# Performance work log

Measured on AMD Instinct MI355X. Metric: run time of the kernel, lower is better.

## Reference

```python
import jax, jax.numpy as jnp
import numpy as np

T, B, I = 64, 128, 512   # seq_len, batch, input_size
H = 512                   # hidden_size
Z = 512                   # zhidden_size (== H required by cell_fn math)
A = 3                     # n_axis
L = 4 + 1                 # n_hidden_layer + 1 levels per Multi_LSTM


def setup_inputs() -> dict:
    key = jax.random.key(0)
    ks = jax.random.split(key, 9)
    s = 0.03  # xavier-ish scale for 512-dim layers
    x = jax.random.normal(ks[0], (T, B, I), jnp.float32)
    # Multi_LSTM cell weights per axis/level: 4 gates (i,f,g,o).
    Wx = jax.random.normal(ks[1], (A, L, 4, H, H), jnp.float32) * s
    Wh = jax.random.normal(ks[2], (A, L, 4, H, H), jnp.float32) * s
    b_lstm = jnp.zeros((A, L, 4, H), jnp.float32)  # b_i + b_h (both init zero)
    # cell_fn (inp_w) weights per level/axis: 3 gates (i,f,c) + combine Wilc.
    Wg_h = jax.random.normal(ks[3], (L, A, 3, Z, H), jnp.float32) * s
    Wg_p = jax.random.normal(ks[4], (L, A, 3, Z, Z), jnp.float32) * s
    bg = jnp.zeros((L, A, 3, Z), jnp.float32)
    Wilc = jax.random.normal(ks[5], (L, A, Z, Z), jnp.float32) * s
    bilc = jnp.zeros((L, A, Z), jnp.float32)
    # single_li: em_size (= L*Z) -> hidden_size
    Wsl = jax.random.normal(ks[6], (H, L * Z), jnp.float32) * s
    bsl = jnp.zeros((H,), jnp.float32)
    # per-timestep linear: hidden_size -> 1 (ModuleList over seq_len)
    Wlin = jax.random.normal(ks[7], (T, 1, H), jnp.float32) * s
    blin = jnp.zeros((T, 1), jnp.float32)
    return dict(x=x, Wx=Wx, Wh=Wh, b_lstm=b_lstm, Wg_h=Wg_h, Wg_p=Wg_p, bg=bg,
                Wilc=Wilc, bilc=bilc, Wsl=Wsl, bsl=bsl, Wlin=Wlin, blin=blin)


def _forward(x, Wx, Wh, b_lstm, Wg_h, Wg_p, bg, Wilc, bilc, Wsl, bsl, Wlin, blin):
    Tn, Bn, _ = x.shape
    An, Ln = Wx.shape[0], Wx.shape[1]
    Hn, Zn = Wx.shape[3], Wilc.shape[2]

    def step(carry, inp_t):
        h_g, hs, cs = carry          # h_g: (B,H); hs,cs: (L,A,B,H)
        xt, wl, bl = inp_t
        # --- per-axis stacked LSTM (Multi_LSTM), levels sequential ---
        inp = jnp.broadcast_to(xt[None], (An, Bn, Hn))
        new_h, new_c = [], []
        for l in range(Ln):
            pre = (jnp.einsum('abi,agoi->abgo', inp, Wx[:, l])
                   + jnp.einsum('abi,agoi->abgo', hs[l], Wh[:, l])
                   + b_lstm[:, l][:, None])           # (A,B,4,H)
            i = jax.nn.sigmoid(pre[:, :, 0]); f = jax.nn.sigmoid(pre[:, :, 1])
            g = jnp.tanh(pre[:, :, 2]);      o = jax.nn.sigmoid(pre[:, :, 3])
            c = f * cs[l] + i * g
            h = o * jnp.tanh(c)
            new_h.append(h); new_c.append(c)
            inp = h
        sh = jnp.stack(new_h)        # (L,A,B,H)
        sc = jnp.stack(new_c)        # (L,A,B,H)
        # --- cell_fn per level, vectorized over levels and axes ---
        pre = (jnp.einsum('bh,lagzh->labgz', h_g, Wg_h)
               + jnp.einsum('labz,lagyz->labgy', sh, Wg_p)
               + bg[:, :, None])                      # (L,A,B,3,Z)
        i = jax.nn.sigmoid(pre[..., 0, :])
        f = jax.nn.sigmoid(pre[..., 1, :])
        g = jnp.tanh(pre[..., 2, :])
        i_cell = i * sc
        c_cell = f * g + i_cell
        # NOTE: torch code uses Wt_1/bt_1 for BOTH t_1 and t_2 (repo bug kept).
        t1 = jnp.einsum('labz,lazy->laby', i_cell, Wilc) + bilc[:, :, None]
        t2 = jnp.einsum('labz,lazy->laby', c_cell, Wilc) + bilc[:, :, None]
        comb = jax.nn.sigmoid(t2.sum(1)) * jax.nn.softmax(t1.sum(1), axis=-1)  # (L,B,Z)
        cat = jnp.transpose(comb, (1, 0, 2)).reshape(Bn, Ln * Zn)
        h_new = cat @ Wsl.T + bsl                      # single_li
        y = h_new @ wl.T + bl                          # per-step linear -> (B,1)
        return (h_new, sh, sc), y

    carry0 = (jnp.zeros((Bn, Hn), x.dtype),
              jnp.zeros((Ln, An, Bn, Hn), x.dtype),
              jnp.zeros((Ln, An, Bn, Hn), x.dtype))
    _, ys = jax.lax.scan(step, carry0, (x, Wlin, blin))
    return ys  # (T,B,1)


def reference(x, Wx, Wh, b_lstm, Wg_h, Wg_p, bg, Wilc, bilc, Wsl, bsl, Wlin, blin):
    return _forward(x, Wx, Wh, b_lstm, Wg_h, Wg_p, bg, Wilc, bilc, Wsl, bsl, Wlin, blin)
```

## Files before the change

kernel.cpp:

```cpp
#include <hip/hip_runtime.h>
#include <cstdint>

typedef __bf16 bf16;
typedef bf16 bf16x8 __attribute__((ext_vector_type(8)));
typedef bf16 bf16x4 __attribute__((ext_vector_type(4)));
typedef float f32x4 __attribute__((ext_vector_type(4)));

#define DI __device__ __forceinline__

DI float sigmoidf_(float x) { return 1.0f / (1.0f + __expf(-x)); }
DI float tanhf_(float x)    { return 1.0f - 2.0f / (__expf(2.0f * x) + 1.0f); }

DI void gld16(const void* g, void* l) {
  __builtin_amdgcn_global_load_lds(
      (const __attribute__((address_space(1))) void*)g,
      (__attribute__((address_space(3))) void*)l, 16, 0, 0);
}

template<int SE>
DI void stage128(char* ldsb, const bf16* act, int k0, int wave, int lane)
{
  const int rsub = lane >> 3, s = lane & 7;
#pragma unroll
  for (int j = 0; j < 4; ++j) {
    const int r = (wave * 4 + j) * 8 + rsub;
    gld16(act + (long)r * SE + k0 + ((s ^ (r & 7)) << 3),
          ldsb + (wave * 4 + j) * 1024);
  }
}

template<int SE>
DI void stage64x2(char* ldsb, const bf16* a1, const bf16* a2, int k0,
                  int wave, int lane)
{
  const int rsub = lane >> 3, s = lane & 7;
#pragma unroll
  for (int j = 0; j < 2; ++j) {
    const int r = (wave * 2 + j) * 8 + rsub;
    const long go = (long)r * SE + k0 + ((s ^ (r & 7)) << 3);
    gld16(a1 + go, ldsb + (wave * 2 + j) * 1024);
    gld16(a2 + go, ldsb + 8192 + (wave * 2 + j) * 1024);
  }
}

DI bf16x8 ldsAf(const char* p, int r, int m)
{
  return *(const bf16x8*)(p + r * 128 + ((m ^ (r & 7)) << 4));
}

template<int NB, int K, int STRIDE>
DI void mmK(f32x4* acc, const bf16* __restrict__ wrow,
            const bf16* __restrict__ act, int q, int col)
{
#pragma unroll
  for (int ki = 0; ki < K / 32; ++ki) {
    const int k = ki * 32 + q * 8;
    bf16x8 wf = *(const bf16x8*)(wrow + k);
#pragma unroll
    for (int bt = 0; bt < NB; ++bt) {
      bf16x8 af = *(const bf16x8*)(act + (long)(bt * 16 + col) * STRIDE + k);
      acc[bt] = __builtin_amdgcn_mfma_f32_16x16x32_bf16(wf, af, acc[bt], 0, 0, 0);
    }
  }
}

DI void d_lstm(int bid, int tid, char* smem,
               const bf16* __restrict__ A0, long a0ss,
               const bf16* __restrict__ A1,
               const bf16* __restrict__ W,
               const float* __restrict__ bias,
               const float* __restrict__ csR,
               float* __restrict__ csW,
               bf16* __restrict__ hOut)
{
  const int bx = bid & 31, ax = bid >> 5;
  const int lane = tid & 63, wave = tid >> 6;
  const int q = lane >> 4, col = lane & 15;
  const int n0 = bx * 64 + wave * 16;
  const bf16* wrow = W + (long)ax * 10485760L + (long)(n0 + col) * 1024;
  const bf16* a0 = A0 + (long)ax * a0ss;
  const bf16* a1 = A1 + (long)ax * 65536;
  f32x4 acc[8] = {};
  stage128<512>(smem, a0, 0, wave, lane);
  __syncthreads();
#pragma unroll 2
  for (int c = 0; c < 16; ++c) {
    if (c < 15) {
      const bf16* an = ((c + 1) < 8) ? a0 : a1;
      stage128<512>(smem + (((c + 1) & 1) << 14), an, ((c + 1) & 7) * 64,
                    wave, lane);
    }
    const char* p = smem + ((c & 1) << 14);
#pragma unroll
    for (int ki = 0; ki < 2; ++ki) {
      bf16x8 wf = *(const bf16x8*)(wrow + c * 64 + ki * 32 + q * 8);
#pragma unroll
      for (int bt = 0; bt < 8; ++bt)
        acc[bt] = __builtin_amdgcn_mfma_f32_16x16x32_bf16(
            wf, ldsAf(p, bt * 16 + col, ki * 4 + q), acc[bt], 0, 0, 0);
    }
    __syncthreads();
  }
  const int o = (n0 >> 2) + q;
  const float* bi = bias + (long)ax * 10240;
  float b0f = bi[o], b1f = bi[512 + o], b2f = bi[1024 + o], b3f = bi[1536 + o];
  const float* csr = csR + (long)ax * 65536;
  float* csw = csW + (long)ax * 65536;
  bf16* hl = hOut + (long)ax * 65536;
#pragma unroll
  for (int bt = 0; bt < 8; ++bt) {
    int b = bt * 16 + col;
    float ig = sigmoidf_(acc[bt][0] + b0f);
    float fg = sigmoidf_(acc[bt][1] + b1f);
    float gg = tanhf_   (acc[bt][2] + b2f);
    float og = sigmoidf_(acc[bt][3] + b3f);
    long idx = (long)b * 512 + o;
    float cn = fg * csr[idx] + ig * gg;
    csw[idx] = cn;
    hl[idx] = (bf16)(og * tanhf_(cn));
  }
}

DI void d_cell(int bid, int tid, char* smem,
               const bf16* __restrict__ hg, const bf16* __restrict__ hsC,
               const bf16* __restrict__ Wg, const float* __restrict__ bgp,
               const float* __restrict__ csC,
               bf16* __restrict__ icat, bf16* __restrict__ ccat)
{
  const int bx = bid & 31, sl = bid >> 5;
  const int l = sl / 3, a = sl - l * 3;
  const int lane = tid & 63, wave = tid >> 6;
  const int q = lane >> 4, col = lane & 15;
  const int n0 = bx * 64 + wave * 16;
  const bf16* wrow = Wg + (long)sl * 2097152L + (long)(n0 + col) * 1024;
  const bf16* a0 = hg;
  const bf16* a1 = hsC + (long)sl * 65536;
  f32x4 acc[8] = {};
  stage128<512>(smem, a0, 0, wave, lane);
  __syncthreads();
#pragma unroll 2
  for (int c = 0; c < 16; ++c) {
    if (c < 15) {
      const bf16* an = ((c + 1) < 8) ? a0 : a1;
      stage128<512>(smem + (((c + 1) & 1) << 14), an, ((c + 1) & 7) * 64,
                    wave, lane);
    }
    const char* p = smem + ((c & 1) << 14);
#pragma unroll
    for (int ki = 0; ki < 2; ++ki) {
      bf16x8 wf = *(const bf16x8*)(wrow + c * 64 + ki * 32 + q * 8);
#pragma unroll
      for (int bt = 0; bt < 8; ++bt)
        acc[bt] = __builtin_amdgcn_mfma_f32_16x16x32_bf16(
            wf, ldsAf(p, bt * 16 + col, ki * 4 + q), acc[bt], 0, 0, 0);
    }
    __syncthreads();
  }
  const int z = (n0 >> 2) + q;
  const float* bgl = bgp + (long)sl * 1536;
  float g0 = bgl[z], g1 = bgl[512 + z], g2 = bgl[1024 + z];
  const float* csl = csC + (long)sl * 65536;
  const long obase = (long)l * 196608 + (long)a * 512 + z;
#pragma unroll
  for (int bt = 0; bt < 8; ++bt) {
    int b = bt * 16 + col;
    float ig = sigmoidf_(acc[bt][0] + g0);
    float fg = sigmoidf_(acc[bt][1] + g1);
    float gg = tanhf_   (acc[bt][2] + g2);
    float sc = csl[(long)b * 512 + z];
    float icl = ig * sc;
    float ccl = fg * gg + icl;
    long oi = obase + (long)b * 1536;
    icat[oi] = (bf16)icl;
    ccat[oi] = (bf16)ccl;
  }
}

DI void d_tg(int bid, int tid, char* smem,
             const bf16* __restrict__ icat, const bf16* __restrict__ ccat,
             const bf16* __restrict__ Wt, const float* __restrict__ bilc,
             float* __restrict__ t1s, float* __restrict__ t2s)
{
  const int bx = bid & 7, by = (bid >> 3) & 1, l = bid >> 4;
  const int lane = tid & 63, wave = tid >> 6;
  const int q = lane >> 4, col = lane & 15;
  const int n0 = bx * 64 + wave * 16;
  const int b0 = by * 64;
  const bf16* wrow = Wt + (long)l * 786432L + (long)(n0 + col) * 1536;
  const bf16* ic = icat + (long)l * 196608 + (long)b0 * 1536;
  const bf16* cc = ccat + (long)l * 196608 + (long)b0 * 1536;
  f32x4 a1[4] = {}, a2[4] = {};
  stage64x2<1536>(smem, ic, cc, 0, wave, lane);
  __syncthreads();
#pragma unroll 2
  for (int c = 0; c < 24; ++c) {
    if (c < 23)
      stage64x2<1536>(smem + (((c + 1) & 1) << 14), ic, cc, (c + 1) * 64,
                      wave, lane);
    const char* p = smem + ((c & 1) << 14);
#pragma unroll
    for (int ki = 0; ki < 2; ++ki) {
      bf16x8 wf = *(const bf16x8*)(wrow + c * 64 + ki * 32 + q * 8);
#pragma unroll
      for (int bt = 0; bt < 4; ++bt) {
        int rl = bt * 16 + col;
        a1[bt] = __builtin_amdgcn_mfma_f32_16x16x32_bf16(
            wf, ldsAf(p, rl, ki * 4 + q), a1[bt], 0, 0, 0);
        a2[bt] = __builtin_amdgcn_mfma_f32_16x16x32_bf16(
            wf, ldsAf(p + 8192, rl, ki * 4 + q), a2[bt], 0, 0, 0);
      }
    }
    __syncthreads();
  }
  const int yb = n0 + 4 * q;
  const float* bl = bilc + (long)l * 1536;
  f32x4 bs;
#pragma unroll
  for (int r = 0; r < 4; ++r) bs[r] = bl[yb + r] + bl[512 + yb + r] + bl[1024 + yb + r];
#pragma unroll
  for (int bt = 0; bt < 4; ++bt) {
    int b = b0 + bt * 16 + col;
    f32x4 v1 = a1[bt] + bs, v2 = a2[bt] + bs;
    *(f32x4*)(t1s + ((long)l * 128 + b) * 512 + yb) = v1;
    *(f32x4*)(t2s + ((long)l * 128 + b) * 512 + yb) = v2;
  }
}

DI void d_comb(int bid, int tid,
               const float* __restrict__ t1s, const float* __restrict__ t2s,
               bf16* __restrict__ cat)
{
  const int bx = bid & 31, l = bid >> 5;
  const int lane = tid & 63, wave = tid >> 6;
  const int b = bx * 4 + wave;
  const float* r1 = t1s + ((long)l * 128 + b) * 512 + lane * 8;
  const float* r2 = t2s + ((long)l * 128 + b) * 512 + lane * 8;
  f32x4 u0 = *(const f32x4*)r1, u1 = *(const f32x4*)(r1 + 4);
  float mx = u0[0];
#pragma unroll
  for (int j = 1; j < 4; ++j) mx = fmaxf(mx, u0[j]);
#pragma unroll
  for (int j = 0; j < 4; ++j) mx = fmaxf(mx, u1[j]);
  for (int d = 32; d > 0; d >>= 1) mx = fmaxf(mx, __shfl_xor(mx, d, 64));
  float e[8], ss = 0.f;
#pragma unroll
  for (int j = 0; j < 4; ++j) { e[j] = __expf(u0[j] - mx); ss += e[j]; }
#pragma unroll
  for (int j = 0; j < 4; ++j) { e[4 + j] = __expf(u1[j] - mx); ss += e[4 + j]; }
  for (int d = 32; d > 0; d >>= 1) ss += __shfl_xor(ss, d, 64);
  float inv = 1.0f / ss;
  f32x4 w0 = *(const f32x4*)r2, w1 = *(const f32x4*)(r2 + 4);
  bf16x8 ob;
#pragma unroll
  for (int j = 0; j < 4; ++j) ob[j]     = (bf16)(sigmoidf_(w0[j]) * e[j]     * inv);
#pragma unroll
  for (int j = 0; j < 4; ++j) ob[4 + j] = (bf16)(sigmoidf_(w1[j]) * e[4 + j] * inv);
  *(bf16x8*)(cat + (long)b * 2560 + l * 512 + lane * 8) = ob;
}

DI void d_slg(int bid, int tid,
              const bf16* __restrict__ cat, const bf16* __restrict__ Wsl,
              float* __restrict__ hnewp)
{
  const int bx = bid & 7, by = (bid >> 3) & 3, kc = bid >> 5;
  const int lane = tid & 63, wave = tid >> 6;
  const int q = lane >> 4, col = lane & 15;
  const int n0 = bx * 64 + wave * 16;
  const int b0 = by * 32;
  const bf16* wrow = Wsl + (long)(n0 + col) * 2560 + kc * 640;
  const bf16* act = cat + kc * 640 + (long)b0 * 2560;
  f32x4 acc[2] = {};
  mmK<2, 640, 2560>(acc, wrow, act, q, col);
  const int nb = n0 + 4 * q;
#pragma unroll
  for (int bt = 0; bt < 2; ++bt) {
    int b = b0 + bt * 16 + col;
    *(f32x4*)(hnewp + ((long)kc * 128 + b) * 512 + nb) = acc[bt];
  }
}

DI void d_fin(int bid, int tid,
              const float* __restrict__ hnewp, const float* __restrict__ bsl,
              const float* __restrict__ wlin, const float* __restrict__ blin,
              bf16* __restrict__ hg, float* __restrict__ out, int t)
{
  const int lane = tid & 63, wave = tid >> 6;
  const int b = bid * 4 + wave;
  const int h0 = lane * 8;
  f32x4 s0 = {0,0,0,0}, s1 = {0,0,0,0};
#pragma unroll
  for (int kc = 0; kc < 4; ++kc) {
    const float* p = hnewp + ((long)kc * 128 + b) * 512 + h0;
    s0 += *(const f32x4*)p;
    s1 += *(const f32x4*)(p + 4);
  }
  s0 += *(const f32x4*)(bsl + h0);
  s1 += *(const f32x4*)(bsl + h0 + 4);
  bf16x8 hb;
#pragma unroll
  for (int j = 0; j < 4; ++j) { hb[j] = (bf16)s0[j]; hb[4 + j] = (bf16)s1[j]; }
  *(bf16x8*)(hg + (long)b * 512 + h0) = hb;
  const float* wl = wlin + (long)t * 512 + h0;
  f32x4 w0 = *(const f32x4*)wl, w1 = *(const f32x4*)(wl + 4);
  float dot = s0[0]*w0[0] + s0[1]*w0[1] + s0[2]*w0[2] + s0[3]*w0[3]
            + s1[0]*w1[0] + s1[1]*w1[1] + s1[2]*w1[2] + s1[3]*w1[3];
  for (int d = 32; d > 0; d >>= 1) dot += __shfl_xor(dot, d, 64);
  if (lane == 0) out[t * 128 + b] = dot + blin[t];
}

#define LSTM_PARAMS const bf16* A0, long a0ss, const bf16* A1, const bf16* W, \
                    const float* bias, const float* csR, float* csW, bf16* hOut
#define LSTM_ARGS   A0, a0ss, A1, W, bias, csR, csW, hOut

__global__ __launch_bounds__(256, 4) void k_f0(int lb, LSTM_PARAMS,
    const bf16* hg, const bf16* hsC, const bf16* Wg, const float* bgp,
    const float* csC, bf16* icat, bf16* ccat)
{
  __shared__ __align__(16) char smem[32768];
  int bid = blockIdx.x;
  if (bid < lb) d_lstm(bid, threadIdx.x, smem, LSTM_ARGS);
  else d_cell(bid - lb, threadIdx.x, smem, hg, hsC, Wg, bgp, csC, icat, ccat);
}

__global__ __launch_bounds__(256, 4) void k_f1(int lb, LSTM_PARAMS,
    const bf16* icat, const bf16* ccat, const bf16* Wt, const float* bilc,
    float* t1s, float* t2s)
{
  __shared__ __align__(16) char smem[32768];
  int bid = blockIdx.x;
  if (bid < lb) d_lstm(bid, threadIdx.x, smem, LSTM_ARGS);
  else d_tg(bid - lb, threadIdx.x, smem, icat, ccat, Wt, bilc, t1s, t2s);
}

__global__ __launch_bounds__(256, 4) void k_f2(int lb, LSTM_PARAMS,
    const float* t1s, const float* t2s, bf16* cat)
{
  __shared__ __align__(16) char smem[32768];
  int bid = blockIdx.x;
  if (bid < lb) d_lstm(bid, threadIdx.x, smem, LSTM_ARGS);
  else d_comb(bid - lb, threadIdx.x, t1s, t2s, cat);
}

__global__ __launch_bounds__(256, 4) void k_f3(int lb, LSTM_PARAMS,
    const bf16* cat, const bf16* Wsl, float* hnp)
{
  __shared__ __align__(16) char smem[32768];
  int bid = blockIdx.x;
  if (bid < lb) d_lstm(bid, threadIdx.x, smem, LSTM_ARGS);
  else d_slg(bid - lb, threadIdx.x, cat, Wsl, hnp);
}

__global__ __launch_bounds__(256, 4) void k_f4(int lb, LSTM_PARAMS,
    const float* hnp, const float* bsl, const float* wlin, const float* blin,
    bf16* hg, float* out, int tc)
{
  __shared__ __align__(16) char smem[32768];
  int bid = blockIdx.x;
  if (bid < lb) d_lstm(bid, threadIdx.x, smem, LSTM_ARGS);
  else d_fin(bid - lb, threadIdx.x, hnp, bsl, wlin, blin, hg, out, tc);
}

__global__ __launch_bounds__(256) void cvt_wxh(const float* __restrict__ Wx,
    const float* __restrict__ Wh, bf16* __restrict__ dst)
{
  long idx = ((long)blockIdx.x * 256 + threadIdx.x) * 4;
  int k = (int)(idx & 1023);
  int n = (int)((idx >> 10) & 2047);
  long al = idx >> 21;
  int g = n & 3, o = n >> 2;
  const float* src = (k < 512)
      ? Wx + ((al * 4 + g) * 512 + o) * 512 + k
      : Wh + ((al * 4 + g) * 512 + o) * 512 + (k - 512);
  f32x4 v = *(const f32x4*)src;
  bf16x4 ov;
#pragma unroll
  for (int j = 0; j < 4; ++j) ov[j] = (bf16)v[j];
  *(bf16x4*)(dst + idx) = ov;
}

__global__ __launch_bounds__(256) void cvt_wg(const float* __restrict__ Wg_h,
    const float* __restrict__ Wg_p, bf16* __restrict__ dst)
{
  long idx = ((long)blockIdx.x * 256 + threadIdx.x) * 4;
  int k = (int)(idx & 1023);
  int n = (int)((idx >> 10) & 2047);
  long la = idx >> 21;
  int g = n & 3, z = n >> 2;
  f32x4 v = {0, 0, 0, 0};
  if (g < 3) {
    const float* src = (k < 512)
        ? Wg_h + ((la * 3 + g) * 512 + z) * 512 + k
        : Wg_p + ((la * 3 + g) * 512 + z) * 512 + (k - 512);
    v = *(const f32x4*)src;
  }
  bf16x4 ov;
#pragma unroll
  for (int j = 0; j < 4; ++j) ov[j] = (bf16)v[j];
  *(bf16x4*)(dst + idx) = ov;
}

__global__ __launch_bounds__(256) void cvt_wt(const float* __restrict__ Wilc,
                                              bf16* __restrict__ dst)
{
  long idx = (long)blockIdx.x * 256 + threadIdx.x;
  int k = (int)(idx % 1536);
  long rest = idx / 1536;
  int y = (int)(rest & 511);
  int l = (int)(rest >> 9);
  int a = k >> 9, z = k & 511;
  dst[idx] = (bf16)Wilc[(((long)l * 3 + a) * 512 + z) * 512 + y];
}

__global__ __launch_bounds__(256) void k_cast(const float* __restrict__ s,
                                              bf16* __restrict__ d)
{
  long i = ((long)blockIdx.x * 256 + threadIdx.x) * 4;
  f32x4 v = *(const f32x4*)(s + i);
  bf16x4 ov;
#pragma unroll
  for (int j = 0; j < 4; ++j) ov[j] = (bf16)v[j];
  *(bf16x4*)(d + i) = ov;
}

__global__ __launch_bounds__(256) void k_zero(uint4* __restrict__ p, long n)
{
  long i = (long)blockIdx.x * 256 + threadIdx.x;
  if (i < n) p[i] = make_uint4(0, 0, 0, 0);
}

extern "C" void kernel_launch(void* const* d_in, const int* in_sizes, int n_in,
                              void* d_out, int out_size, void* d_ws, size_t ws_size,
                              hipStream_t stream)
{
  const float* x    = (const float*)d_in[0];
  const float* Wx   = (const float*)d_in[1];
  const float* Wh   = (const float*)d_in[2];
  const float* b_l  = (const float*)d_in[3];
  const float* Wg_h = (const float*)d_in[4];
  const float* Wg_p = (const float*)d_in[5];
  const float* bg   = (const float*)d_in[6];
  const float* Wilc = (const float*)d_in[7];
  const float* bilc = (const float*)d_in[8];
  const float* Wsl  = (const float*)d_in[9];
  const float* bsl  = (const float*)d_in[10];
  const float* Wlin = (const float*)d_in[11];
  const float* blin = (const float*)d_in[12];
  float* out = (float*)d_out;

  char* w = (char*)d_ws;
  auto alloc = [&](long bytes) { char* p = w; w += (bytes + 255) & ~255L; return p; };
  bf16* Wcat = (bf16*)alloc(31457280L * 2);
  bf16* Wg   = (bf16*)alloc(31457280L * 2);
  bf16* Wt   = (bf16*)alloc(3932160L * 2);
  bf16* Wslb = (bf16*)alloc(1310720L * 2);
  bf16* xbf  = (bf16*)alloc(4194304L * 2);
  char* zbase = w;
  bf16* hs0  = (bf16*)alloc(983040L * 2);
  bf16* hs1  = (bf16*)alloc(983040L * 2);
  bf16* hgb  = (bf16*)alloc(65536L * 2);
  float* cs0 = (float*)alloc(983040L * 4);
  float* cs1 = (float*)alloc(983040L * 4);
  long zbytes = w - zbase;
  bf16* icat = (bf16*)alloc(983040L * 2);
  bf16* ccat = (bf16*)alloc(983040L * 2);
  float* t1s = (float*)alloc(327680L * 4);
  float* t2s = (float*)alloc(327680L * 4);
  bf16* catb = (bf16*)alloc(327680L * 2);
  float* hnp = (float*)alloc(262144L * 4);
  (void)ws_size; (void)n_in; (void)in_sizes; (void)out_size;

  cvt_wxh<<<30720, 256, 0, stream>>>(Wx, Wh, Wcat);
  cvt_wg <<<30720, 256, 0, stream>>>(Wg_h, Wg_p, Wg);
  cvt_wt <<<15360, 256, 0, stream>>>(Wilc, Wt);
  k_cast <<<1280,  256, 0, stream>>>(Wsl, Wslb);
  k_cast <<<4096,  256, 0, stream>>>(x, xbf);
  {
    long n16 = zbytes / 16;
    k_zero<<<(int)((n16 + 255) / 256), 256, 0, stream>>>((uint4*)zbase, n16);
  }

  for (int s = 0; s < 65; ++s) {
    const int t  = (s < 64) ? s : 63;
    const int tc = (s > 0) ? s - 1 : 0;
    const int lb = (s < 64) ? 96 : 0;
    const int cb0 = (s > 0) ? 480 : 0, cb1 = (s > 0) ? 80 : 0,
              cb2 = (s > 0) ? 160 : 0, cb3 = (s > 0) ? 128 : 0,
              cb4 = (s > 0) ? 32 : 0;
    const bf16*  hsR = (t & 1) ? hs1 : hs0;
    bf16*        hsW = (t & 1) ? hs0 : hs1;
    const float* csR = (t & 1) ? cs1 : cs0;
    float*       csW = (t & 1) ? cs0 : cs1;
    const bf16*  hsC = (tc & 1) ? hs0 : hs1;
    const float* csC = (tc & 1) ? cs0 : cs1;

#define LA(l) ((l) == 0 ? xbf + (long)t * 65536 : hsW + (long)((l) - 1) * 196608), \
              ((l) == 0 ? 0L : 65536L), \
              hsR + (long)(l) * 196608, Wcat + (long)(l) * 2097152, \
              b_l + (long)(l) * 2048, csR + (long)(l) * 196608, \
              csW + (long)(l) * 196608, hsW + (long)(l) * 196608

    k_f0<<<lb + cb0, 256, 0, stream>>>(lb, LA(0), hgb, hsC, Wg, bg, csC, icat, ccat);
    k_f1<<<lb + cb1, 256, 0, stream>>>(lb, LA(1), icat, ccat, Wt, bilc, t1s, t2s);
    k_f2<<<lb + cb2, 256, 0, stream>>>(lb, LA(2), t1s, t2s, catb);
    k_f3<<<lb + cb3, 256, 0, stream>>>(lb, LA(3), catb, Wslb, hnp);
    k_f4<<<lb + cb4, 256, 0, stream>>>(lb, LA(4), hnp, bsl, Wlin, blin, hgb, out, tc);
#undef LA
  }
}
```

Baseline: 7.887 ms.

## Replace per-stage kernel launches with one persistent kernel and grid barriers

```diff
diff --git a/kernel.cpp b/kernel.cpp
--- a/kernel.cpp
+++ b/kernel.cpp
@@ -308,56 +308,110 @@
   if (lane == 0) out[t * 128 + b] = dot + blin[t];
 }
 
-#define LSTM_PARAMS const bf16* A0, long a0ss, const bf16* A1, const bf16* W, \
-                    const float* bias, const float* csR, float* csW, bf16* hOut
-#define LSTM_ARGS   A0, a0ss, A1, W, bias, csR, csW, hOut
-
-__global__ __launch_bounds__(256, 4) void k_f0(int lb, LSTM_PARAMS,
-    const bf16* hg, const bf16* hsC, const bf16* Wg, const float* bgp,
-    const float* csC, bf16* icat, bf16* ccat)
+DI void gsync(unsigned* bar, int bid, unsigned target)
+{
+  __syncthreads();
+  if (threadIdx.x == 0) {
+    __threadfence();
+    unsigned o = __hip_atomic_fetch_add(&bar[(bid & 7) * 32], 1u,
+                     __ATOMIC_ACQ_REL, __HIP_MEMORY_SCOPE_AGENT);
+    if ((o & 63u) == 63u) {
+      unsigned r = __hip_atomic_fetch_add(&bar[256], 1u,
+                       __ATOMIC_ACQ_REL, __HIP_MEMORY_SCOPE_AGENT);
+      if ((r & 7u) == 7u)
+        __hip_atomic_fetch_add(&bar[288], 1u,
+            __ATOMIC_ACQ_REL, __HIP_MEMORY_SCOPE_AGENT);
+    }
+    while (__hip_atomic_load(&bar[288], __ATOMIC_RELAXED,
+                             __HIP_MEMORY_SCOPE_AGENT) < target)
+      __builtin_amdgcn_s_sleep(2);
+    __threadfence();
+  }
+  __syncthreads();
+}
+
+struct KArgs {
+  const bf16 *xbf, *Wcat, *Wg, *Wt, *Wslb;
+  const float *b_l, *bg, *bilc, *bsl, *Wlin, *blin;
+  bf16 *hs0, *hs1, *hgb, *icat, *ccat, *catb;
+  float *cs0, *cs1, *t1s, *t2s, *hnp, *out;
+  unsigned *bar;
+};
+
+__global__ __launch_bounds__(256, 2) void k_main(KArgs A)
 {
   __shared__ __align__(16) char smem[32768];
-  int bid = blockIdx.x;
-  if (bid < lb) d_lstm(bid, threadIdx.x, smem, LSTM_ARGS);
-  else d_cell(bid - lb, threadIdx.x, smem, hg, hsC, Wg, bgp, csC, icat, ccat);
-}
-
-__global__ __launch_bounds__(256, 4) void k_f1(int lb, LSTM_PARAMS,
-    const bf16* icat, const bf16* ccat, const bf16* Wt, const float* bilc,
-    float* t1s, float* t2s)
-{
-  __shared__ __align__(16) char smem[32768];
-  int bid = blockIdx.x;
-  if (bid < lb) d_lstm(bid, threadIdx.x, smem, LSTM_ARGS);
-  else d_tg(bid - lb, threadIdx.x, smem, icat, ccat, Wt, bilc, t1s, t2s);
-}
-
-__global__ __launch_bounds__(256, 4) void k_f2(int lb, LSTM_PARAMS,
-    const float* t1s, const float* t2s, bf16* cat)
-{
-  __shared__ __align__(16) char smem[32768];
-  int bid = blockIdx.x;
-  if (bid < lb) d_lstm(bid, threadIdx.x, smem, LSTM_ARGS);
-  else d_comb(bid - lb, threadIdx.x, t1s, t2s, cat);
-}
-
-__global__ __launch_bounds__(256, 4) void k_f3(int lb, LSTM_PARAMS,
-    const bf16* cat, const bf16* Wsl, float* hnp)
-{
-  __shared__ __align__(16) char smem[32768];
-  int bid = blockIdx.x;
-  if (bid < lb) d_lstm(bid, threadIdx.x, smem, LSTM_ARGS);
-  else d_slg(bid - lb, threadIdx.x, cat, Wsl, hnp);
-}
-
-__global__ __launch_bounds__(256, 4) void k_f4(int lb, LSTM_PARAMS,
-    const float* hnp, const float* bsl, const float* wlin, const float* blin,
-    bf16* hg, float* out, int tc)
-{
-  __shared__ __align__(16) char smem[32768];
-  int bid = blockIdx.x;
-  if (bid < lb) d_lstm(bid, threadIdx.x, smem, LSTM_ARGS);
-  else d_fin(bid - lb, threadIdx.x, hnp, bsl, wlin, blin, hg, out, tc);
+  const int bid = blockIdx.x;
+  const int tid = threadIdx.x;
+  unsigned round = 0;
+
+  for (int s = 0; s < 65; ++s) {
+    const int t  = (s < 64) ? s : 63;
+    const int tc = s - 1;
+    const int ln = (s < 64) ? 96 : 0;
+    const bf16*  hsR = (t & 1) ? A.hs1 : A.hs0;
+    bf16*        hsW = (t & 1) ? A.hs0 : A.hs1;
+    const float* csR = (t & 1) ? A.cs1 : A.cs0;
+    float*       csW = (t & 1) ? A.cs0 : A.cs1;
+    const bf16*  hsC = (tc & 1) ? A.hs0 : A.hs1;
+    const float* csC = (tc & 1) ? A.cs0 : A.cs1;
+
+#define LSTM_L(l, task) d_lstm(task, tid, smem, \
+      ((l) == 0 ? A.xbf + (long)t * 65536 : (const bf16*)(hsW + (long)((l)-1) * 196608)), \
+      ((l) == 0 ? 0L : 65536L), \
+      hsR + (long)(l) * 196608, A.Wcat + (long)(l) * 2097152, \
+      A.b_l + (long)(l) * 2048, csR + (long)(l) * 196608, \
+      csW + (long)(l) * 196608, hsW + (long)(l) * 196608)
+
+    {
+      const int tot = ln + ((s > 0) ? 480 : 0);
+      if (bid < tot) {
+        if (bid < ln) LSTM_L(0, bid);
+        else d_cell(bid - ln, tid, smem, A.hgb, hsC, A.Wg, A.bg, csC,
+                    A.icat, A.ccat);
+      }
+      const int t2 = 1023 - bid;
+      if (t2 >= 512 && t2 < tot)
+        d_cell(t2 - ln, tid, smem, A.hgb, hsC, A.Wg, A.bg, csC,
+               A.icat, A.ccat);
+      gsync(A.bar, bid, ++round);
+    }
+    {
+      const int tot = ln + ((s > 0) ? 80 : 0);
+      if (bid < tot) {
+        if (bid < ln) LSTM_L(1, bid);
+        else d_tg(bid - ln, tid, smem, A.icat, A.ccat, A.Wt, A.bilc,
+                  A.t1s, A.t2s);
+      }
+      gsync(A.bar, bid, ++round);
+    }
+    {
+      const int tot = ln + ((s > 0) ? 160 : 0);
+      if (bid < tot) {
+        if (bid < ln) LSTM_L(2, bid);
+        else d_comb(bid - ln, tid, A.t1s, A.t2s, A.catb);
+      }
+      gsync(A.bar, bid, ++round);
+    }
+    {
+      const int tot = ln + ((s > 0) ? 128 : 0);
+      if (bid < tot) {
+        if (bid < ln) LSTM_L(3, bid);
+        else d_slg(bid - ln, tid, A.catb, A.Wslb, A.hnp);
+      }
+      gsync(A.bar, bid, ++round);
+    }
+    {
+      const int tot = ln + ((s > 0) ? 32 : 0);
+      if (bid < tot) {
+        if (bid < ln) LSTM_L(4, bid);
+        else d_fin(bid - ln, tid, A.hnp, A.bsl, A.Wlin, A.blin, A.hgb,
+                   A.out, tc);
+      }
+      gsync(A.bar, bid, ++round);
+    }
+#undef LSTM_L
+  }
 }
 
 __global__ __launch_bounds__(256) void cvt_wxh(const float* __restrict__ Wx,
@@ -460,6 +514,7 @@
   bf16* hgb  = (bf16*)alloc(65536L * 2);
   float* cs0 = (float*)alloc(983040L * 4);
   float* cs1 = (float*)alloc(983040L * 4);
+  unsigned* bar = (unsigned*)alloc(1536);
   long zbytes = w - zbase;
   bf16* icat = (bf16*)alloc(983040L * 2);
   bf16* ccat = (bf16*)alloc(983040L * 2);
@@ -479,31 +534,11 @@
     k_zero<<<(int)((n16 + 255) / 256), 256, 0, stream>>>((uint4*)zbase, n16);
   }
 
-  for (int s = 0; s < 65; ++s) {
-    const int t  = (s < 64) ? s : 63;
-    const int tc = (s > 0) ? s - 1 : 0;
-    const int lb = (s < 64) ? 96 : 0;
-    const int cb0 = (s > 0) ? 480 : 0, cb1 = (s > 0) ? 80 : 0,
-              cb2 = (s > 0) ? 160 : 0, cb3 = (s > 0) ? 128 : 0,
-              cb4 = (s > 0) ? 32 : 0;
-    const bf16*  hsR = (t & 1) ? hs1 : hs0;
-    bf16*        hsW = (t & 1) ? hs0 : hs1;
-    const float* csR = (t & 1) ? cs1 : cs0;
-    float*       csW = (t & 1) ? cs0 : cs1;
-    const bf16*  hsC = (tc & 1) ? hs0 : hs1;
-    const float* csC = (tc & 1) ? cs0 : cs1;
-
-#define LA(l) ((l) == 0 ? xbf + (long)t * 65536 : hsW + (long)((l) - 1) * 196608), \
-              ((l) == 0 ? 0L : 65536L), \
-              hsR + (long)(l) * 196608, Wcat + (long)(l) * 2097152, \
-              b_l + (long)(l) * 2048, csR + (long)(l) * 196608, \
-              csW + (long)(l) * 196608, hsW + (long)(l) * 196608
-
-    k_f0<<<lb + cb0, 256, 0, stream>>>(lb, LA(0), hgb, hsC, Wg, bg, csC, icat, ccat);
-    k_f1<<<lb + cb1, 256, 0, stream>>>(lb, LA(1), icat, ccat, Wt, bilc, t1s, t2s);
-    k_f2<<<lb + cb2, 256, 0, stream>>>(lb, LA(2), t1s, t2s, catb);
-    k_f3<<<lb + cb3, 256, 0, stream>>>(lb, LA(3), catb, Wslb, hnp);
-    k_f4<<<lb + cb4, 256, 0, stream>>>(lb, LA(4), hnp, bsl, Wlin, blin, hgb, out, tc);
-#undef LA
-  }
-}
+  KArgs A;
+  A.xbf = xbf; A.Wcat = Wcat; A.Wg = Wg; A.Wt = Wt; A.Wslb = Wslb;
+  A.b_l = b_l; A.bg = bg; A.bilc = bilc; A.bsl = bsl; A.Wlin = Wlin; A.blin = blin;
+  A.hs0 = hs0; A.hs1 = hs1; A.hgb = hgb; A.icat = icat; A.ccat = ccat; A.catb = catb;
+  A.cs0 = cs0; A.cs1 = cs1; A.t1s = t1s; A.t2s = t2s; A.hnp = hnp; A.out = out;
+  A.bar = bar;
+  k_main<<<512, 256, 0, stream>>>(A);
+}
```

Result: slower. 19.67 ms (+149.4%).
